# Optimization experiments

Measured on AMD Instinct MI355X. Metric: run time of the kernel, lower is better.

The kernel has to match this reference:

```python
import jax, jax.numpy as jnp
import numpy as np

NUM_HEADS = 8
SCALE = 1.0
BN_EPS = 1e-5


def _mlp1d(x, W1, g1, b1, W2):
    # Conv1d(k=1, bias=False) -> BatchNorm1d (training-mode batch stats) -> ReLU -> Conv1d(k=1, bias=False)
    h = jnp.einsum('oi,bil->bol', W1, x)
    mu = h.mean(axis=(0, 2), keepdims=True)
    var = h.var(axis=(0, 2), keepdims=True)  # biased var, as torch BN training
    h = (h - mu) * jax.lax.rsqrt(var + BN_EPS)
    h = jax.nn.relu(h * g1[None, :, None] + b1[None, :, None])
    return jnp.einsum('oi,bil->bol', W2, h)


def setup_inputs() -> dict:
    key = jax.random.key(0)
    ks = jax.random.split(key, 8)
    b, c, hh, ww = 64, 2048, 14, 14
    hid, out = 4096, 256
    d = {'x': jax.random.normal(ks[0], (b, c, hh, ww), jnp.float32)}

    def w(k, o, i):
        return jax.random.normal(k, (o, i), jnp.float32) * np.float32(1.0 / np.sqrt(i))

    i = 1
    for pre in ('p', 'pp', 'po'):  # proj, proj_pixel, proj_obj
        d[pre + 'W1'] = w(ks[i], hid, c); i += 1
        d[pre + 'G1'] = jnp.ones((hid,), jnp.float32)
        d[pre + 'B1'] = jnp.zeros((hid,), jnp.float32)
        d[pre + 'W2'] = w(ks[i], out, hid); i += 1
    return d


def reference(x, pW1, pG1, pB1, pW2, ppW1, ppG1, ppB1, ppW2, poW1, poG1, poB1, poW2):
    b, c, h, w = x.shape
    xf = x.reshape(b, c, h * w)                      # flatten(2)
    x_pool = xf.mean(axis=2, keepdims=True)          # adaptive_avg_pool2d(x, 1)
    z_g = _mlp1d(x_pool, pW1, pG1, pB1, pW2)         # [b, 256, 1]
    z_feat = _mlp1d(xf, ppW1, ppG1, ppB1, ppW2)      # [b, 256, hw]
    # F.normalize(dim=1) with eps=1e-12, then /scale
    nrm = jnp.maximum(jnp.linalg.norm(z_feat, axis=1, keepdims=True), 1e-12)
    attn = (z_feat / nrm) / SCALE
    attn = attn.reshape(b, NUM_HEADS, -1, h * w)     # [b, nh, 256/nh, hw]
    attn = jax.nn.softmax(attn, axis=-1)
    x4 = xf.reshape(b, NUM_HEADS, c // NUM_HEADS, h * w)
    # torch.matmul(x, obj_attn.transpose(3, 2)) : [b,nh,c/nh,hw] @ [b,nh,hw,q]
    obj_val = jnp.einsum('bnkl,bnql->bnkq', x4, attn).reshape(b, c, -1)  # [b, c, 256/nh]
    obj_val = _mlp1d(obj_val, poW1, poG1, poB1, poW2)                    # [b, 256, 32]
    return z_g, obj_val
```

## Files before the change

### kernel.cpp

```cpp
#include <hip/hip_runtime.h>
#include <hip/hip_bf16.h>

using bf16 = __hip_bfloat16;
typedef __bf16 bf16x8v __attribute__((ext_vector_type(8)));
typedef float f32x4 __attribute__((ext_vector_type(4)));

#define BN_EPS 1e-5f

__device__ __forceinline__ void stval(float* p, float v) { *p = v; }
__device__ __forceinline__ void stval(bf16* p, float v)  { *p = __float2bfloat16(v); }

__device__ __forceinline__ void gload_lds16(const void* g, void* l) {
    __builtin_amdgcn_global_load_lds(
        (const __attribute__((address_space(1))) unsigned int*)g,
        (__attribute__((address_space(3))) unsigned int*)l,
        16, 0, 0);
}

__device__ __forceinline__ int xcd_swz(int orig, int nwg) {
    int q = nwg >> 3, r = nwg & 7;
    int xcd = orig & 7, idx = orig >> 3;
    return (xcd < r ? xcd * (q + 1) : r * (q + 1) + (xcd - r) * q) + idx;
}

template<typename TC>
__global__ __launch_bounds__(512, 2) void mfma_tn8(
    const bf16* __restrict__ A, const bf16* __restrict__ B, TC* __restrict__ C,
    int M, int N, int K, float* __restrict__ ps, float* __restrict__ pq)
{
    __shared__ char lds[131072];
    const int NT = K >> 6;
    const int tid = threadIdx.x;
    const int lane = tid & 63;
    const int wv = tid >> 6;
    const int wm = wv >> 2;
    const int wn = wv & 3;

    const int nbx = gridDim.x;
    int flat = blockIdx.y * nbx + blockIdx.x;
    const int cpx = (nbx * gridDim.y) >> 3;
    flat = (flat & 7) * cpx + (flat >> 3);
    const int mtile = flat / nbx;
    const long m0 = (long)mtile * 256;
    const long n0 = (long)(flat % nbx) * 256;

    const int trow = tid >> 3;
    const int ks = (((tid & 7) ^ ((tid >> 3) & 7)) << 3);
    const bf16* Arow0 = A + (m0 + trow) * (long)K + ks;
    const bf16* Brow0 = B + (n0 + trow) * (long)K + ks;
    char* ldsA = (char*)lds + tid * 16;
    char* ldsB = (char*)lds + 32768 + tid * 16;

    auto stage_a = [&](int bbuf, int kt) {
        const bf16* g = Arow0 + ((long)kt << 6);
        char* d = ldsA + (bbuf << 16);
        gload_lds16(g, d);
        gload_lds16(g + ((long)K << 6),  d + 8192);
        gload_lds16(g + ((long)K << 7),  d + 16384);
        gload_lds16(g + 192L * (long)K,  d + 24576);
    };
    auto stage_b = [&](int bbuf, int kt) {
        const bf16* g = Brow0 + ((long)kt << 6);
        char* d = ldsB + (bbuf << 16);
        gload_lds16(g, d);
        gload_lds16(g + ((long)K << 6),  d + 8192);
        gload_lds16(g + ((long)K << 7),  d + 16384);
        gload_lds16(g + 192L * (long)K,  d + 24576);
    };

    const int fr = lane & 15, fc = lane >> 4;
    const int ca0 = ((fc ^ (fr & 7)) << 4);
    const int ca1 = (((4 + fc) ^ (fr & 7)) << 4);

    f32x4 acc[8][4];
#pragma unroll
    for (int m = 0; m < 8; ++m)
#pragma unroll
        for (int n = 0; n < 4; ++n) acc[m][n] = (f32x4){0.f, 0.f, 0.f, 0.f};

    stage_a(0, 0); stage_b(0, 0); stage_a(1, 1); stage_b(1, 1);

    for (int T = 0; T < NT; ++T) {
        const int bb = T & 1;
        const char* Ard = (const char*)lds + (bb << 16) + (wm * 128 + fr) * 128;
        const char* Brd = (const char*)lds + (bb << 16) + 32768 + (wn * 64 + fr) * 128;

        if (T == 0)          { asm volatile("s_waitcnt vmcnt(8)" ::: "memory"); }
        else if (T < NT - 1) { asm volatile("s_waitcnt vmcnt(4)" ::: "memory"); }
        else                 { asm volatile("s_waitcnt vmcnt(0)" ::: "memory"); }
        __builtin_amdgcn_s_barrier();
        __builtin_amdgcn_sched_barrier(0);

        bf16x8v a0[8], a1[8];
#pragma unroll
        for (int m = 0; m < 8; ++m) {
            a0[m] = *(const bf16x8v*)(Ard + m * 2048 + ca0);
            a1[m] = *(const bf16x8v*)(Ard + m * 2048 + ca1);
        }
        bf16x8v b00 = *(const bf16x8v*)(Brd + ca0);
        bf16x8v b01 = *(const bf16x8v*)(Brd + ca1);
        bf16x8v b10 = *(const bf16x8v*)(Brd + 2048 + ca0);
        bf16x8v b11 = *(const bf16x8v*)(Brd + 2048 + ca1);

        if (T >= 1 && T + 1 < NT) stage_b(bb ^ 1, T + 1);

        __builtin_amdgcn_s_setprio(1);
#pragma unroll
        for (int m = 0; m < 8; ++m) {
            acc[m][0] = __builtin_amdgcn_mfma_f32_16x16x32_bf16(a0[m], b00, acc[m][0], 0, 0, 0);
            acc[m][0] = __builtin_amdgcn_mfma_f32_16x16x32_bf16(a1[m], b01, acc[m][0], 0, 0, 0);
            acc[m][1] = __builtin_amdgcn_mfma_f32_16x16x32_bf16(a0[m], b10, acc[m][1], 0, 0, 0);
            acc[m][1] = __builtin_amdgcn_mfma_f32_16x16x32_bf16(a1[m], b11, acc[m][1], 0, 0, 0);
        }
        __builtin_amdgcn_s_setprio(0);

        __builtin_amdgcn_s_barrier();
        __builtin_amdgcn_sched_barrier(0);

        bf16x8v b20 = *(const bf16x8v*)(Brd + 2 * 2048 + ca0);
        bf16x8v b21 = *(const bf16x8v*)(Brd + 2 * 2048 + ca1);
        bf16x8v b30 = *(const bf16x8v*)(Brd + 3 * 2048 + ca0);
        bf16x8v b31 = *(const bf16x8v*)(Brd + 3 * 2048 + ca1);

        if (T + 2 < NT) stage_a(bb, T + 2);

        __builtin_amdgcn_s_setprio(1);
#pragma unroll
        for (int m = 0; m < 8; ++m) {
            acc[m][2] = __builtin_amdgcn_mfma_f32_16x16x32_bf16(a0[m], b20, acc[m][2], 0, 0, 0);
            acc[m][2] = __builtin_amdgcn_mfma_f32_16x16x32_bf16(a1[m], b21, acc[m][2], 0, 0, 0);
            acc[m][3] = __builtin_amdgcn_mfma_f32_16x16x32_bf16(a0[m], b30, acc[m][3], 0, 0, 0);
            acc[m][3] = __builtin_amdgcn_mfma_f32_16x16x32_bf16(a1[m], b31, acc[m][3], 0, 0, 0);
        }
        __builtin_amdgcn_s_setprio(0);
    }

#pragma unroll
    for (int m = 0; m < 8; ++m) {
        long gr = m0 + wm * 128 + m * 16 + fc * 4;
#pragma unroll
        for (int n = 0; n < 4; ++n) {
            long gc = n0 + wn * 64 + n * 16 + fr;
            TC* cp = C + gr * N + gc;
#pragma unroll
            for (int r = 0; r < 4; ++r) stval(cp + (long)r * N, acc[m][n][r]);
        }
    }

    if (ps != nullptr) {
        __syncthreads();
        float* red = (float*)lds;
        float cs[4], cq[4];
#pragma unroll
        for (int n = 0; n < 4; ++n) {
            float s = 0.f, q = 0.f;
#pragma unroll
            for (int m = 0; m < 8; ++m)
#pragma unroll
                for (int r = 0; r < 4; ++r) {
                    float v = __bfloat162float(__float2bfloat16(acc[m][n][r]));
                    s += v; q += v * v;
                }
            s += __shfl_xor(s, 16, 64); s += __shfl_xor(s, 32, 64);
            q += __shfl_xor(q, 16, 64); q += __shfl_xor(q, 32, 64);
            cs[n] = s; cq[n] = q;
        }
        if (fc == 0) {
#pragma unroll
            for (int n = 0; n < 4; ++n) {
                red[wv * 64 + n * 16 + fr] = cs[n];
                red[512 + wv * 64 + n * 16 + fr] = cq[n];
            }
        }
        __syncthreads();
        if (tid < 256) {
            int c = tid, wnn = c >> 6, idx = c & 63;
            float s = red[wnn * 64 + idx] + red[(4 + wnn) * 64 + idx];
            float q = red[512 + wnn * 64 + idx] + red[512 + (4 + wnn) * 64 + idx];
            ps[(long)mtile * N + n0 + c] = s;
            pq[(long)mtile * N + n0 + c] = q;
        }
    }
}

template<typename TC>
__global__ __launch_bounds__(256) void mfma_tn(
    const bf16* __restrict__ A, const bf16* __restrict__ B, TC* __restrict__ C,
    int M, int N, int K, float* __restrict__ ps, float* __restrict__ pq)
{
    __shared__ alignas(16) unsigned short As[128 * 32];
    __shared__ alignas(16) unsigned short Bs[128 * 32];

    const int tid = threadIdx.x;
    const int l = tid & 63;
    const int nwg = gridDim.x * gridDim.y;
    int s = xcd_swz(blockIdx.y * gridDim.x + blockIdx.x, nwg);
    const int by = s / gridDim.x, bx = s % gridDim.x;
    const long m0 = (long)by * 128;
    const long n0 = (long)bx * 128;
    const int wr = (tid >> 7) & 1;
    const int wc = (tid >> 6) & 1;

    const int off0 = tid * 16;
    const int row0 = off0 >> 6;
    const int kp0  = (off0 >> 4) & 3;
    const bf16* Ag0 = A + (m0 + row0) * (long)K + kp0 * 8;
    const bf16* Ag1 = A + (m0 + row0 + 64) * (long)K + kp0 * 8;
    const bf16* Bg0 = B + (n0 + row0) * (long)K + kp0 * 8;
    const bf16* Bg1 = B + (n0 + row0 + 64) * (long)K + kp0 * 8;
    char* Asl0 = (char*)As + off0;
    char* Asl1 = (char*)As + off0 + 4096;
    char* Bsl0 = (char*)Bs + off0;
    char* Bsl1 = (char*)Bs + off0 + 4096;

    f32x4 acc[4][4];
#pragma unroll
    for (int m = 0; m < 4; ++m)
#pragma unroll
        for (int n = 0; n < 4; ++n) acc[m][n] = (f32x4){0.f, 0.f, 0.f, 0.f};

    const int fr = l & 15;
    const int fc = l >> 4;
    int aoff[4], boff[4];
#pragma unroll
    for (int m = 0; m < 4; ++m) aoff[m] = ((wr * 64 + m * 16 + fr) * 4 + fc) * 16;
#pragma unroll
    for (int n = 0; n < 4; ++n) boff[n] = ((wc * 64 + n * 16 + fr) * 4 + fc) * 16;

    for (int k0 = 0; k0 < K; k0 += 32) {
        gload_lds16(Ag0 + k0, Asl0);
        gload_lds16(Ag1 + k0, Asl1);
        gload_lds16(Bg0 + k0, Bsl0);
        gload_lds16(Bg1 + k0, Bsl1);
        __syncthreads();

        bf16x8v af[4], bfr[4];
#pragma unroll
        for (int m = 0; m < 4; ++m) af[m]  = *(const bf16x8v*)((const char*)As + aoff[m]);
#pragma unroll
        for (int n = 0; n < 4; ++n) bfr[n] = *(const bf16x8v*)((const char*)Bs + boff[n]);
#pragma unroll
        for (int m = 0; m < 4; ++m)
#pragma unroll
            for (int n = 0; n < 4; ++n)
                acc[m][n] = __builtin_amdgcn_mfma_f32_16x16x32_bf16(af[m], bfr[n], acc[m][n], 0, 0, 0);
        __syncthreads();
    }

#pragma unroll
    for (int m = 0; m < 4; ++m) {
        long gr = m0 + wr * 64 + m * 16 + fc * 4;
#pragma unroll
        for (int n = 0; n < 4; ++n) {
            long gc = n0 + wc * 64 + n * 16 + fr;
            TC* cp = C + gr * N + gc;
#pragma unroll
            for (int r = 0; r < 4; ++r) stval(cp + (long)r * N, acc[m][n][r]);
        }
    }

    if (ps != nullptr) {
        float* red = (float*)As;
        float cs[4], cq[4];
#pragma unroll
        for (int n = 0; n < 4; ++n) {
            float s2 = 0.f, q2 = 0.f;
#pragma unroll
            for (int m = 0; m < 4; ++m)
#pragma unroll
                for (int r = 0; r < 4; ++r) {
                    float v = __bfloat162float(__float2bfloat16(acc[m][n][r]));
                    s2 += v; q2 += v * v;
                }
            s2 += __shfl_xor(s2, 16, 64); s2 += __shfl_xor(s2, 32, 64);
            q2 += __shfl_xor(q2, 16, 64); q2 += __shfl_xor(q2, 32, 64);
            cs[n] = s2; cq[n] = q2;
        }
        if (fc == 0) {
#pragma unroll
            for (int n = 0; n < 4; ++n) {
                int c = wc * 64 + n * 16 + fr;
                red[wr * 128 + c] = cs[n];
                red[256 + wr * 128 + c] = cq[n];
            }
        }
        __syncthreads();
        if (tid < 128) {
            float sv = red[tid] + red[128 + tid];
            float qv = red[256 + tid] + red[384 + tid];
            ps[(long)by * N + n0 + tid] = sv;
            pq[(long)by * N + n0 + tid] = qv;
        }
    }
}

__global__ __launch_bounds__(256) void mfma_tn_skbn(
    const bf16* __restrict__ A, const bf16* __restrict__ B, float* __restrict__ Cp,
    int M, int N, int K, int KCH, const float* __restrict__ ta, const float* __restrict__ tc)
{
    __shared__ alignas(16) unsigned short As[128 * 32];
    __shared__ alignas(16) unsigned short Bs[128 * 32];

    const int tid = threadIdx.x;
    const int l = tid & 63;
    const int gxy = gridDim.x * gridDim.y;
    const int nwg = gxy * gridDim.z;
    int s = xcd_swz((blockIdx.z * gridDim.y + blockIdx.y) * gridDim.x + blockIdx.x, nwg);
    const int bz = s / gxy;
    const int rem = s % gxy;
    const int by = rem / gridDim.x, bx = rem % gridDim.x;
    const long m0 = (long)by * 128;
    const long n0 = (long)bx * 128;
    const int wr = (tid >> 7) & 1;
    const int wc = (tid >> 6) & 1;
    const int ksrt = bz * KCH;

    const int off0 = tid * 16;
    const int row0 = off0 >> 6;
    const int kp0  = (off0 >> 4) & 3;
    const bf16* Ag0 = A + (m0 + row0) * (long)K + kp0 * 8 + ksrt;
    const bf16* Ag1 = A + (m0 + row0 + 64) * (long)K + kp0 * 8 + ksrt;
    const bf16* Bg0 = B + (n0 + row0) * (long)K + kp0 * 8 + ksrt;
    const bf16* Bg1 = B + (n0 + row0 + 64) * (long)K + kp0 * 8 + ksrt;
    char* Asl0 = (char*)As + off0;
    char* Asl1 = (char*)As + off0 + 4096;
    char* Bsl0 = (char*)Bs + off0;
    char* Bsl1 = (char*)Bs + off0 + 4096;

    f32x4 acc[4][4];
#pragma unroll
    for (int m = 0; m < 4; ++m)
#pragma unroll
        for (int n = 0; n < 4; ++n) acc[m][n] = (f32x4){0.f, 0.f, 0.f, 0.f};

    const int fr = l & 15;
    const int fc = l >> 4;
    int aoff[4], boff[4];
#pragma unroll
    for (int m = 0; m < 4; ++m) aoff[m] = ((wr * 64 + m * 16 + fr) * 4 + fc) * 16;
#pragma unroll
    for (int n = 0; n < 4; ++n) boff[n] = ((wc * 64 + n * 16 + fr) * 4 + fc) * 16;

    for (int k0 = 0; k0 < KCH; k0 += 32) {
        gload_lds16(Bg0 + k0, Bsl0);
        gload_lds16(Bg1 + k0, Bsl1);

        union { bf16 h[8]; uint4 u; } r0, r1;
        r0.u = *(const uint4*)(Ag0 + k0);
        r1.u = *(const uint4*)(Ag1 + k0);
        const int kb = ksrt + k0 + kp0 * 8;
        float4 av0 = *(const float4*)(ta + kb);
        float4 av1 = *(const float4*)(ta + kb + 4);
        float4 cv0 = *(const float4*)(tc + kb);
        float4 cv1 = *(const float4*)(tc + kb + 4);
        float av[8] = {av0.x, av0.y, av0.z, av0.w, av1.x, av1.y, av1.z, av1.w};
        float cv[8] = {cv0.x, cv0.y, cv0.z, cv0.w, cv1.x, cv1.y, cv1.z, cv1.w};
#pragma unroll
        for (int j = 0; j < 8; ++j) {
            float v = fmaxf(fmaf(av[j], __bfloat162float(r0.h[j]), cv[j]), 0.f);
            r0.h[j] = __float2bfloat16(v);
            v = fmaxf(fmaf(av[j], __bfloat162float(r1.h[j]), cv[j]), 0.f);
            r1.h[j] = __float2bfloat16(v);
        }
        *(uint4*)Asl0 = r0.u;
        *(uint4*)Asl1 = r1.u;
        __syncthreads();

        bf16x8v af[4], bfr[4];
#pragma unroll
        for (int m = 0; m < 4; ++m) af[m]  = *(const bf16x8v*)((const char*)As + aoff[m]);
#pragma unroll
        for (int n = 0; n < 4; ++n) bfr[n] = *(const bf16x8v*)((const char*)Bs + boff[n]);
#pragma unroll
        for (int m = 0; m < 4; ++m)
#pragma unroll
            for (int n = 0; n < 4; ++n)
                acc[m][n] = __builtin_amdgcn_mfma_f32_16x16x32_bf16(af[m], bfr[n], acc[m][n], 0, 0, 0);
        __syncthreads();
    }

    float* Cb = Cp + (long)bz * M * N;
#pragma unroll
    for (int m = 0; m < 4; ++m) {
        long gr = m0 + wr * 64 + m * 16 + fc * 4;
#pragma unroll
        for (int n = 0; n < 4; ++n) {
            long gc = n0 + wc * 64 + n * 16 + fr;
            float* cp = Cb + gr * N + gc;
#pragma unroll
            for (int r = 0; r < 4; ++r) cp[(long)r * N] = acc[m][n][r];
        }
    }
}

__global__ __launch_bounds__(256) void objmm_k(
    const bf16* __restrict__ attnP, const bf16* __restrict__ xP, bf16* __restrict__ objinT)
{
    __shared__ alignas(16) unsigned short As[32 * 32];
    __shared__ alignas(16) unsigned short Bs[256 * 32];
    const int tid = threadIdx.x, lane = tid & 63, wv = tid >> 6;
    const int b = blockIdx.x >> 3, h = blockIdx.x & 7;
    const bf16* Ab = attnP + ((long)(b * 256 + h * 32)) * 224;
    const bf16* Bb = xP + ((long)(b * 2048 + h * 256)) * 224;
    const int fr = lane & 15, fc = lane >> 4;
    const int srow = tid >> 2, schk = tid & 3;

    f32x4 acc[2][4];
#pragma unroll
    for (int m = 0; m < 2; ++m)
#pragma unroll
        for (int n = 0; n < 4; ++n) acc[m][n] = (f32x4){0.f, 0.f, 0.f, 0.f};

    for (int k0 = 0; k0 < 224; k0 += 32) {
        if (wv < 2)
            gload_lds16(Ab + (long)srow * 224 + schk * 8 + k0, (char*)As + tid * 16);
#pragma unroll
        for (int j = 0; j < 4; ++j)
            gload_lds16(Bb + (long)(j * 64 + srow) * 224 + schk * 8 + k0,
                        (char*)Bs + j * 4096 + tid * 16);
        __syncthreads();

        bf16x8v af[2], bfr[4];
#pragma unroll
        for (int m = 0; m < 2; ++m)
            af[m] = *(const bf16x8v*)((const char*)As + (m * 16 + fr) * 64 + fc * 16);
#pragma unroll
        for (int n = 0; n < 4; ++n)
            bfr[n] = *(const bf16x8v*)((const char*)Bs + (wv * 64 + n * 16 + fr) * 64 + fc * 16);
#pragma unroll
        for (int m = 0; m < 2; ++m)
#pragma unroll
            for (int n = 0; n < 4; ++n)
                acc[m][n] = __builtin_amdgcn_mfma_f32_16x16x32_bf16(af[m], bfr[n], acc[m][n], 0, 0, 0);
        __syncthreads();
    }

#pragma unroll
    for (int m = 0; m < 2; ++m) {
        long gr = (long)b * 32 + m * 16 + fc * 4;
#pragma unroll
        for (int n = 0; n < 4; ++n) {
            long gc = (long)h * 256 + wv * 64 + n * 16 + fr;
            bf16* cp = objinT + gr * 2048 + gc;
#pragma unroll
            for (int r = 0; r < 4; ++r) cp[(long)r * 2048] = __float2bfloat16(acc[m][n][r]);
        }
    }
}

__global__ __launch_bounds__(256) void foldnorm_k(const float* __restrict__ p,
    float* __restrict__ z, float* __restrict__ invn)
{
    int j = blockIdx.x * 4 + (threadIdx.x >> 6);
    int lane = threadIdx.x & 63;
    long off = (long)j * 256 + lane * 4;
    float4 a = *(const float4*)(p + off);
    float4 b = *(const float4*)(p + 3211264L + off);
    float4 c = *(const float4*)(p + 2 * 3211264L + off);
    float4 d = *(const float4*)(p + 3 * 3211264L + off);
    float4 s;
    s.x = (a.x + b.x) + (c.x + d.x);
    s.y = (a.y + b.y) + (c.y + d.y);
    s.z = (a.z + b.z) + (c.z + d.z);
    s.w = (a.w + b.w) + (c.w + d.w);
    *(float4*)(z + off) = s;
    float q = s.x * s.x + s.y * s.y + s.z * s.z + s.w * s.w;
#pragma unroll
    for (int off2 = 32; off2; off2 >>= 1) q += __shfl_xor(q, off2, 64);
    if (lane == 0) invn[j] = 1.f / fmaxf(sqrtf(q), 1e-12f);
}

__global__ __launch_bounds__(256) void foldout_k(const float* __restrict__ p, float* __restrict__ out)
{
    int o = blockIdx.x * 256 + threadIdx.x;
    int b = o >> 13, rem = o & 8191, q = rem >> 5, tt = rem & 31;
    long base = ((long)(b * 32 + tt)) * 256 + q;
    float s = 0.f;
#pragma unroll
    for (int z = 0; z < 8; ++z) s += p[(long)z * 524288 + base];
    out[o] = s;
}

__global__ __launch_bounds__(256) void convert4_k(
    const float* __restrict__ w1, const float* __restrict__ w2,
    const float* __restrict__ w3, const float* __restrict__ w4,
    bf16* __restrict__ o1, bf16* __restrict__ o2,
    bf16* __restrict__ o3, bf16* __restrict__ o4)
{
    const long L1 = 8388608, L2 = 1048576;
    long i = ((long)blockIdx.x * 256 + threadIdx.x) * 8;
    const float* src; bf16* dst; long e;
    if (i < L1)                { src = w1; dst = o1; e = i; }
    else if (i < L1 + L2)      { src = w2; dst = o2; e = i - L1; }
    else if (i < 2*L1 + L2)    { src = w3; dst = o3; e = i - L1 - L2; }
    else if (i < 2*L1 + 2*L2)  { src = w4; dst = o4; e = i - 2*L1 - L2; }
    else return;
    float4 v0 = *(const float4*)(src + e);
    float4 v1 = *(const float4*)(src + e + 4);
    union { bf16 h[8]; uint4 u; } r;
    r.h[0] = __float2bfloat16(v0.x); r.h[1] = __float2bfloat16(v0.y);
    r.h[2] = __float2bfloat16(v0.z); r.h[3] = __float2bfloat16(v0.w);
    r.h[4] = __float2bfloat16(v1.x); r.h[5] = __float2bfloat16(v1.y);
    r.h[6] = __float2bfloat16(v1.z); r.h[7] = __float2bfloat16(v1.w);
    *(uint4*)(dst + e) = r.u;
}

__global__ __launch_bounds__(256) void packx2_k(const float* __restrict__ x,
    bf16* __restrict__ XT, bf16* __restrict__ xP, float* __restrict__ xpT)
{
    __shared__ unsigned short tile[196 * 66 + 4];
    __shared__ float pp[64];
    const int t = threadIdx.x;
    const int b = blockIdx.y, c0 = blockIdx.x * 64;
    const int wvi = t >> 6, lane = t & 63;

    for (int p = 0; p < 16; ++p) {
        int c = p * 4 + wvi;
        const float* row = x + ((long)b * 2048 + c0 + c) * 196;
        float v0 = row[lane];
        float v1 = row[lane + 64];
        float v2 = row[lane + 128];
        float v3 = (lane < 4) ? row[lane + 192] : 0.f;
        bf16 h0 = __float2bfloat16(v0);
        bf16 h1 = __float2bfloat16(v1);
        bf16 h2 = __float2bfloat16(v2);
        bf16 h3 = __float2bfloat16(v3);
        tile[lane * 66 + c]         = *(unsigned short*)&h0;
        tile[(lane + 64) * 66 + c]  = *(unsigned short*)&h1;
        tile[(lane + 128) * 66 + c] = *(unsigned short*)&h2;
        if (lane < 4) tile[(lane + 192) * 66 + c] = *(unsigned short*)&h3;
        float s = v0 + v1 + v2 + v3;
#pragma unroll
        for (int off = 32; off; off >>= 1) s += __shfl_xor(s, off, 64);
        if (lane == 0) pp[c] = s;
    }
    __syncthreads();
    if (t < 64) xpT[(c0 + t) * 64 + b] = pp[t] * (1.f / 196.f);

    for (int u = t; u < 196 * 8; u += 256) {
        int l = u >> 3, cc = u & 7;
        const unsigned short* sp = &tile[l * 66 + cc * 8];
        uint4 r;
        r.x = *(const unsigned int*)(sp);
        r.y = *(const unsigned int*)(sp + 2);
        r.z = *(const unsigned int*)(sp + 4);
        r.w = *(const unsigned int*)(sp + 6);
        *(uint4*)(&XT[((long)b * 196 + l) * 2048 + c0 + cc * 8]) = r;
    }

    for (int u = t; u < 64 * 28; u += 256) {
        int c = u / 28, ch = u % 28;
        int l0 = ch * 8;
        union { unsigned short h[8]; uint4 v; } r;
#pragma unroll
        for (int e = 0; e < 8; ++e) {
            int ll = l0 + e;
            r.h[e] = (ll < 196) ? tile[ll * 66 + c] : (unsigned short)0;
        }
        *(uint4*)(xP + ((long)b * 2048 + c0 + c) * 224 + l0) = r.v;
    }
}

__global__ __launch_bounds__(256) void colstat2_k(const float* __restrict__ ps, const float* __restrict__ pq,
    int P, float invN, const float* __restrict__ g, const float* __restrict__ be,
    float* __restrict__ ta, float* __restrict__ tc)
{
    int c = blockIdx.x * 256 + threadIdx.x;
    float s = 0.f, q = 0.f;
    for (int p = 0; p < P; ++p) { s += ps[(long)p * 4096 + c]; q += pq[(long)p * 4096 + c]; }
    float mu  = s * invN;
    float var = q * invN - mu * mu;
    float a   = g[c] * rsqrtf(var + BN_EPS);
    ta[c] = a;
    tc[c] = be[c] - mu * a;
}

__global__ __launch_bounds__(256) void softmax2_k(const float* __restrict__ z,
    const float* __restrict__ invn, bf16* __restrict__ attnP)
{
    int row  = blockIdx.x * 4 + (threadIdx.x >> 6);
    int lane = threadIdx.x & 63;
    int b = row >> 8, q = row & 255;
    float v[4];
    float mx = -INFINITY;
#pragma unroll
    for (int i = 0; i < 4; ++i) {
        int l = lane + 64 * i;
        if (l < 196) {
            int j = b * 196 + l;
            v[i] = z[(long)j * 256 + q] * invn[j];
        } else v[i] = -INFINITY;
        mx = fmaxf(mx, v[i]);
    }
#pragma unroll
    for (int off = 32; off; off >>= 1) mx = fmaxf(mx, __shfl_xor(mx, off, 64));
    float s = 0.f;
#pragma unroll
    for (int i = 0; i < 4; ++i) {
        v[i] = (lane + 64 * i < 196) ? __expf(v[i] - mx) : 0.f;
        s += v[i];
    }
#pragma unroll
    for (int off = 32; off; off >>= 1) s += __shfl_xor(s, off, 64);
    float is = 1.f / s;
    bf16* rp = attnP + (long)row * 224;
#pragma unroll
    for (int i = 0; i < 4; ++i) {
        int l = lane + 64 * i;
        if (l < 196) rp[l] = __float2bfloat16(v[i] * is);
        else if (l < 224) rp[l] = __float2bfloat16(0.f);
    }
}

template<bool TRANS>
__global__ __launch_bounds__(256) void gemmsk_k(
    const float* __restrict__ A, const float* __restrict__ B, float* __restrict__ Cp,
    int M, int N, int K, int lda, int ldbk, int KCH,
    const float* __restrict__ tra, const float* __restrict__ trc)
{
    constexpr int BM = 64, BN = 64, BK = 16;
    __shared__ float As[BK][BM + 4];
    __shared__ float Bs[BK][BN + 4];

    const int tid = threadIdx.x;
    const int m0 = blockIdx.y * BM;
    const int ks = blockIdx.z * KCH;
    const int ke = min(K, ks + KCH);

    const int tIdm = tid / 16;
    const int tIdn = tid % 16;
    const int aK  = tid % BK;
    const int aM0 = tid / BK;
    const int bN  = tid % BN;
    const int bK0 = tid / BN;

    float acc[4][4];
#pragma unroll
    for (int u = 0; u < 4; ++u)
#pragma unroll
        for (int v = 0; v < 4; ++v) acc[u][v] = 0.f;

    for (int k0 = ks; k0 < ke; k0 += BK) {
#pragma unroll
        for (int i = 0; i < 4; ++i) {
            int m = aM0 + 16 * i;
            int gk = k0 + aK, gm = m0 + m;
            float v = 0.f;
            if (gk < ke && gm < M) v = A[(long)gm * lda + gk];
            As[aK][m] = v;
        }
#pragma unroll
        for (int i = 0; i < 4; ++i) {
            int kk = bK0 + 4 * i;
            int gk = k0 + kk;
            float v = 0.f;
            if (gk < ke && bN < N) {
                v = B[(long)gk * ldbk + bN];
                if (TRANS) v = fmaxf(tra[gk] * v + trc[gk], 0.f);
            }
            Bs[kk][bN] = v;
        }
        __syncthreads();
#pragma unroll
        for (int kk = 0; kk < BK; ++kk) {
            float a[4], b[4];
#pragma unroll
            for (int u = 0; u < 4; ++u) a[u] = As[kk][tIdm * 4 + u];
#pragma unroll
            for (int v = 0; v < 4; ++v) b[v] = Bs[kk][tIdn * 4 + v];
#pragma unroll
            for (int u = 0; u < 4; ++u)
#pragma unroll
                for (int v = 0; v < 4; ++v)
                    acc[u][v] = fmaf(a[u], b[v], acc[u][v]);
        }
        __syncthreads();
    }

    float* Cb = Cp + (long)blockIdx.z * M * N;
#pragma unroll
    for (int u = 0; u < 4; ++u) {
        int gm = m0 + tIdm * 4 + u;
        if (gm >= M) continue;
#pragma unroll
        for (int v = 0; v < 4; ++v) {
            int gn = tIdn * 4 + v;
            if (gn < N) Cb[(long)gm * N + gn] = acc[u][v];
        }
    }
}

__global__ __launch_bounds__(256) void skbn_k(const float* __restrict__ Cp,
    const float* __restrict__ g, const float* __restrict__ be,
    float* __restrict__ h1, float* __restrict__ ta, float* __restrict__ tc)
{
    int o = blockIdx.x * 4 + (threadIdx.x >> 6);
    int b = threadIdx.x & 63;
    float s = 0.f;
#pragma unroll
    for (int p = 0; p < 16; ++p) s += Cp[(long)p * 262144 + o * 64 + b];
    h1[o * 64 + b] = s;
    float s1 = s, s2 = s * s;
#pragma unroll
    for (int off = 32; off; off >>= 1) {
        s1 += __shfl_down(s1, off, 64);
        s2 += __shfl_down(s2, off, 64);
    }
    if (b == 0) {
        float mu  = s1 * (1.f / 64.f);
        float var = s2 * (1.f / 64.f) - mu * mu;
        float a   = g[o] * rsqrtf(var + BN_EPS);
        ta[o] = a;
        tc[o] = be[o] - mu * a;
    }
}

__global__ __launch_bounds__(256) void skreduce_k(const float* __restrict__ Cp, int P, long MN,
    int Nn, int ldm, int ldn, float* __restrict__ out)
{
    long i = (long)blockIdx.x * 256 + threadIdx.x;
    if (i >= MN) return;
    float s = 0.f;
    for (int p = 0; p < P; ++p) s += Cp[(long)p * MN + i];
    int m = (int)(i / Nn), n = (int)(i % Nn);
    out[(long)m * ldm + (long)n * ldn] = s;
}

extern "C" void kernel_launch(void* const* d_in, const int* in_sizes, int n_in,
                              void* d_out, int out_size, void* d_ws, size_t ws_size,
                              hipStream_t stream)
{
    const float* x    = (const float*)d_in[0];
    const float* pW1  = (const float*)d_in[1];
    const float* pG1  = (const float*)d_in[2];
    const float* pB1  = (const float*)d_in[3];
    const float* pW2  = (const float*)d_in[4];
    const float* ppW1 = (const float*)d_in[5];
    const float* ppG1 = (const float*)d_in[6];
    const float* ppB1 = (const float*)d_in[7];
    const float* ppW2 = (const float*)d_in[8];
    const float* poW1 = (const float*)d_in[9];
    const float* poG1 = (const float*)d_in[10];
    const float* poB1 = (const float*)d_in[11];
    const float* poW2 = (const float*)d_in[12];
    float* out = (float*)d_out;
    (void)in_sizes; (void)n_in; (void)out_size; (void)ws_size;

    char* w = (char*)d_ws;
    auto alloc = [&](size_t bytes) -> char* {
        char* p = w; w += (bytes + 255) & ~(size_t)255; return p;
    };
    bf16* ppW1b = (bf16*)alloc((size_t)4096 * 2048 * 2);
    bf16* ppW2b = (bf16*)alloc((size_t)256 * 4096 * 2);
    bf16* poW1b = (bf16*)alloc((size_t)4096 * 2048 * 2);
    bf16* poW2b = (bf16*)alloc((size_t)256 * 4096 * 2);
    char* region1 = alloc((size_t)12544 * 2048 * 2);
    bf16*  XT     = (bf16*)region1;
    float* skpG2  = (float*)region1;
    bf16*  attnP  = (bf16*)region1;
    bf16*  objinT = (bf16*)(region1 + 12845056);
    bf16*  hobjT  = (bf16*)(region1 + 12845056 + 8388608);
    bf16* xP     = (bf16*)alloc((size_t)64 * 2048 * 224 * 2);
    bf16* hfeatT = (bf16*)alloc((size_t)12544 * 4096 * 2);
    float* zfeatT = (float*)alloc((size_t)12544 * 256 * 4);
    float* ps    = (float*)alloc((size_t)49 * 4096 * 4);
    float* pq    = (float*)alloc((size_t)49 * 4096 * 4);
    float* invn  = (float*)alloc((size_t)12544 * 4);
    float* a2    = (float*)alloc(4096 * 4);
    float* c2    = (float*)alloc(4096 * 4);
    float* a3    = (float*)alloc(4096 * 4);
    float* c3    = (float*)alloc(4096 * 4);
    float* xpT   = (float*)alloc((size_t)2048 * 64 * 4);
    float* h1    = (float*)alloc((size_t)4096 * 64 * 4);
    float* a1    = (float*)alloc(4096 * 4);
    float* c1    = (float*)alloc(4096 * 4);
    float* skp1  = (float*)alloc((size_t)16 * 4096 * 64 * 4);
    float* skp2  = (float*)alloc((size_t)32 * 256 * 64 * 4);
    float* skp5  = (float*)alloc((size_t)8 * 2048 * 256 * 4);

    convert4_k<<<9216, 256, 0, stream>>>(ppW1, ppW2, poW1, poW2, ppW1b, ppW2b, poW1b, poW2b);
    packx2_k<<<dim3(32, 64), 256, 0, stream>>>(x, XT, xP, xpT);

    gemmsk_k<false><<<dim3(1, 64, 16), 256, 0, stream>>>(
        pW1, xpT, skp1, 4096, 64, 2048, 2048, 64, 128, nullptr, nullptr);
    skbn_k<<<1024, 256, 0, stream>>>(skp1, pG1, pB1, h1, a1, c1);
    gemmsk_k<true><<<dim3(1, 4, 32), 256, 0, stream>>>(
        pW2, h1, skp2, 256, 64, 4096, 4096, 64, 128, a1, c1);
    skreduce_k<<<64, 256, 0, stream>>>(skp2, 32, (long)256 * 64, 64, 1, 256, out);

    mfma_tn8<bf16><<<dim3(16, 49), 512, 0, stream>>>(XT, ppW1b, hfeatT, 12544, 4096, 2048, ps, pq);
    colstat2_k<<<16, 256, 0, stream>>>(ps, pq, 49, 1.f / 12544.f, ppG1, ppB1, a2, c2);

    mfma_tn_skbn<<<dim3(2, 98, 4), 256, 0, stream>>>(
        hfeatT, ppW2b, skpG2, 12544, 256, 4096, 1024, a2, c2);
    foldnorm_k<<<3136, 256, 0, stream>>>(skpG2, zfeatT, invn);

    softmax2_k<<<4096, 256, 0, stream>>>(zfeatT, invn, attnP);

    objmm_k<<<512, 256, 0, stream>>>(attnP, xP, objinT);

    mfma_tn<bf16><<<dim3(32, 16), 256, 0, stream>>>(objinT, poW1b, hobjT, 2048, 4096, 2048, ps, pq);
    colstat2_k<<<16, 256, 0, stream>>>(ps, pq, 16, 1.f / 2048.f, poG1, poB1, a3, c3);

    mfma_tn_skbn<<<dim3(2, 16, 8), 256, 0, stream>>>(
        hobjT, poW2b, skp5, 2048, 256, 4096, 512, a3, c3);
    foldout_k<<<2048, 256, 0, stream>>>(skp5, out + 16384);
}
```

Measured before the change: 613.0 us.

## Split GEMM main loop into four quadrant phases with half-tile prefetch

Restructures the 256x256 MFMA GEMM inner loop into four phases, each working on half of the A rows and half of the B columns. Global-to-LDS prefetches are issued in half-tile chunks between phases, and barriers with waitcnt sit at each phase. Only half of the A fragments are held in registers at a time, which lowers register pressure. The intent is finer interleaving of memory traffic with MFMA work, at the cost of more barriers per iteration and a more complex hazard schedule that needs correct double-buffer synchronisation.

```diff
diff --git a/kernel.cpp b/kernel.cpp
--- a/kernel.cpp
+++ b/kernel.cpp
@@ -22,6 +22,8 @@
     int xcd = orig & 7, idx = orig >> 3;
     return (xcd < r ? xcd * (q + 1) : r * (q + 1) + (xcd - r) * q) + idx;
 }
+
+#define MFMA_BF16 __builtin_amdgcn_mfma_f32_16x16x32_bf16
 
 template<typename TC>
 __global__ __launch_bounds__(512, 2) void mfma_tn8(
@@ -51,21 +53,17 @@
     char* ldsA = (char*)lds + tid * 16;
     char* ldsB = (char*)lds + 32768 + tid * 16;
 
-    auto stage_a = [&](int bbuf, int kt) {
-        const bf16* g = Arow0 + ((long)kt << 6);
-        char* d = ldsA + (bbuf << 16);
+    auto stage_a_half = [&](int bbuf, int kt, int h) {
+        const bf16* g = Arow0 + (long)(h * 64) * K + ((long)kt << 6);
+        char* d = ldsA + (bbuf << 16) + h * 8192;
         gload_lds16(g, d);
-        gload_lds16(g + ((long)K << 6),  d + 8192);
-        gload_lds16(g + ((long)K << 7),  d + 16384);
-        gload_lds16(g + 192L * (long)K,  d + 24576);
+        gload_lds16(g + ((long)K << 7), d + 16384);
     };
-    auto stage_b = [&](int bbuf, int kt) {
-        const bf16* g = Brow0 + ((long)kt << 6);
-        char* d = ldsB + (bbuf << 16);
+    auto stage_b_half = [&](int bbuf, int kt, int h) {
+        const bf16* g = Brow0 + (long)(h * 128) * K + ((long)kt << 6);
+        char* d = ldsB + (bbuf << 16) + h * 16384;
         gload_lds16(g, d);
-        gload_lds16(g + ((long)K << 6),  d + 8192);
-        gload_lds16(g + ((long)K << 7),  d + 16384);
-        gload_lds16(g + 192L * (long)K,  d + 24576);
+        gload_lds16(g + ((long)K << 6), d + 8192);
     };
 
     const int fr = lane & 15, fc = lane >> 4;
@@ -78,61 +76,98 @@
 #pragma unroll
         for (int n = 0; n < 4; ++n) acc[m][n] = (f32x4){0.f, 0.f, 0.f, 0.f};
 
-    stage_a(0, 0); stage_b(0, 0); stage_a(1, 1); stage_b(1, 1);
+    stage_a_half(0, 0, 0); stage_a_half(0, 0, 1);
+    stage_b_half(0, 0, 0); stage_b_half(0, 0, 1);
+    stage_a_half(1, 1, 0); stage_a_half(1, 1, 1);
+    asm volatile("s_waitcnt vmcnt(4)" ::: "memory");
+    __builtin_amdgcn_s_barrier();
+    __builtin_amdgcn_sched_barrier(0);
 
     for (int T = 0; T < NT; ++T) {
         const int bb = T & 1;
         const char* Ard = (const char*)lds + (bb << 16) + (wm * 128 + fr) * 128;
         const char* Brd = (const char*)lds + (bb << 16) + 32768 + (wn * 64 + fr) * 128;
 
-        if (T == 0)          { asm volatile("s_waitcnt vmcnt(8)" ::: "memory"); }
-        else if (T < NT - 1) { asm volatile("s_waitcnt vmcnt(4)" ::: "memory"); }
-        else                 { asm volatile("s_waitcnt vmcnt(0)" ::: "memory"); }
+        bf16x8v a0[4], a1[4];
+        bf16x8v b00, b01, b10, b11, b20, b21, b30, b31;
+
+#pragma unroll
+        for (int i = 0; i < 4; ++i) {
+            a0[i] = *(const bf16x8v*)(Ard + i * 2048 + ca0);
+            a1[i] = *(const bf16x8v*)(Ard + i * 2048 + ca1);
+        }
+        b00 = *(const bf16x8v*)(Brd + ca0);
+        b01 = *(const bf16x8v*)(Brd + ca1);
+        b10 = *(const bf16x8v*)(Brd + 2048 + ca0);
+        b11 = *(const bf16x8v*)(Brd + 2048 + ca1);
+        if (T + 1 < NT) stage_b_half(bb ^ 1, T + 1, 0);
+        __builtin_amdgcn_s_barrier();
+        asm volatile("s_waitcnt lgkmcnt(0)" ::: "memory");
+        __builtin_amdgcn_sched_barrier(0);
+        __builtin_amdgcn_s_setprio(1);
+#pragma unroll
+        for (int i = 0; i < 4; ++i) {
+            acc[i][0] = MFMA_BF16(a0[i], b00, acc[i][0], 0, 0, 0);
+            acc[i][0] = MFMA_BF16(a1[i], b01, acc[i][0], 0, 0, 0);
+            acc[i][1] = MFMA_BF16(a0[i], b10, acc[i][1], 0, 0, 0);
+            acc[i][1] = MFMA_BF16(a1[i], b11, acc[i][1], 0, 0, 0);
+        }
+        __builtin_amdgcn_s_setprio(0);
+        __builtin_amdgcn_s_barrier();
+
+        b20 = *(const bf16x8v*)(Brd + 2 * 2048 + ca0);
+        b21 = *(const bf16x8v*)(Brd + 2 * 2048 + ca1);
+        b30 = *(const bf16x8v*)(Brd + 3 * 2048 + ca0);
+        b31 = *(const bf16x8v*)(Brd + 3 * 2048 + ca1);
+        if (T + 1 < NT) stage_b_half(bb ^ 1, T + 1, 1);
+        __builtin_amdgcn_s_barrier();
+        asm volatile("s_waitcnt lgkmcnt(0)" ::: "memory");
+        __builtin_amdgcn_sched_barrier(0);
+        __builtin_amdgcn_s_setprio(1);
+#pragma unroll
+        for (int i = 0; i < 4; ++i) {
+            acc[i][2] = MFMA_BF16(a0[i], b20, acc[i][2], 0, 0, 0);
+            acc[i][2] = MFMA_BF16(a1[i], b21, acc[i][2], 0, 0, 0);
+            acc[i][3] = MFMA_BF16(a0[i], b30, acc[i][3], 0, 0, 0);
+            acc[i][3] = MFMA_BF16(a1[i], b31, acc[i][3], 0, 0, 0);
+        }
+        __builtin_amdgcn_s_setprio(0);
+        __builtin_amdgcn_s_barrier();
+
+#pragma unroll
+        for (int i = 0; i < 4; ++i) {
+            a0[i] = *(const bf16x8v*)(Ard + (4 + i) * 2048 + ca0);
+            a1[i] = *(const bf16x8v*)(Ard + (4 + i) * 2048 + ca1);
+        }
+        if (T + 2 < NT) stage_a_half(bb, T + 2, 0);
+        __builtin_amdgcn_s_barrier();
+        asm volatile("s_waitcnt lgkmcnt(0)" ::: "memory");
+        __builtin_amdgcn_sched_barrier(0);
+        __builtin_amdgcn_s_setprio(1);
+#pragma unroll
+        for (int i = 0; i < 4; ++i) {
+            acc[4 + i][0] = MFMA_BF16(a0[i], b00, acc[4 + i][0], 0, 0, 0);
+            acc[4 + i][0] = MFMA_BF16(a1[i], b01, acc[4 + i][0], 0, 0, 0);
+            acc[4 + i][1] = MFMA_BF16(a0[i], b10, acc[4 + i][1], 0, 0, 0);
+            acc[4 + i][1] = MFMA_BF16(a1[i], b11, acc[4 + i][1], 0, 0, 0);
+        }
+        __builtin_amdgcn_s_setprio(0);
+        __builtin_amdgcn_s_barrier();
+
+        if (T + 2 < NT) stage_a_half(bb, T + 2, 1);
+        __builtin_amdgcn_s_setprio(1);
+#pragma unroll
+        for (int i = 0; i < 4; ++i) {
+            acc[4 + i][2] = MFMA_BF16(a0[i], b20, acc[4 + i][2], 0, 0, 0);
+            acc[4 + i][2] = MFMA_BF16(a1[i], b21, acc[4 + i][2], 0, 0, 0);
+            acc[4 + i][3] = MFMA_BF16(a0[i], b30, acc[4 + i][3], 0, 0, 0);
+            acc[4 + i][3] = MFMA_BF16(a1[i], b31, acc[4 + i][3], 0, 0, 0);
+        }
+        __builtin_amdgcn_s_setprio(0);
+        if (T + 2 < NT)      { asm volatile("s_waitcnt vmcnt(4)" ::: "memory"); }
+        else if (T + 1 < NT) { asm volatile("s_waitcnt vmcnt(0)" ::: "memory"); }
         __builtin_amdgcn_s_barrier();
         __builtin_amdgcn_sched_barrier(0);
-
-        bf16x8v a0[8], a1[8];
-#pragma unroll
-        for (int m = 0; m < 8; ++m) {
-            a0[m] = *(const bf16x8v*)(Ard + m * 2048 + ca0);
-            a1[m] = *(const bf16x8v*)(Ard + m * 2048 + ca1);
-        }
-        bf16x8v b00 = *(const bf16x8v*)(Brd + ca0);
-        bf16x8v b01 = *(const bf16x8v*)(Brd + ca1);
-        bf16x8v b10 = *(const bf16x8v*)(Brd + 2048 + ca0);
-        bf16x8v b11 = *(const bf16x8v*)(Brd + 2048 + ca1);
-
-        if (T >= 1 && T + 1 < NT) stage_b(bb ^ 1, T + 1);
-
-        __builtin_amdgcn_s_setprio(1);
-#pragma unroll
-        for (int m = 0; m < 8; ++m) {
-            acc[m][0] = __builtin_amdgcn_mfma_f32_16x16x32_bf16(a0[m], b00, acc[m][0], 0, 0, 0);
-            acc[m][0] = __builtin_amdgcn_mfma_f32_16x16x32_bf16(a1[m], b01, acc[m][0], 0, 0, 0);
-            acc[m][1] = __builtin_amdgcn_mfma_f32_16x16x32_bf16(a0[m], b10, acc[m][1], 0, 0, 0);
-            acc[m][1] = __builtin_amdgcn_mfma_f32_16x16x32_bf16(a1[m], b11, acc[m][1], 0, 0, 0);
-        }
-        __builtin_amdgcn_s_setprio(0);
-
-        __builtin_amdgcn_s_barrier();
-        __builtin_amdgcn_sched_barrier(0);
-
-        bf16x8v b20 = *(const bf16x8v*)(Brd + 2 * 2048 + ca0);
-        bf16x8v b21 = *(const bf16x8v*)(Brd + 2 * 2048 + ca1);
-        bf16x8v b30 = *(const bf16x8v*)(Brd + 3 * 2048 + ca0);
-        bf16x8v b31 = *(const bf16x8v*)(Brd + 3 * 2048 + ca1);
-
-        if (T + 2 < NT) stage_a(bb, T + 2);
-
-        __builtin_amdgcn_s_setprio(1);
-#pragma unroll
-        for (int m = 0; m < 8; ++m) {
-            acc[m][2] = __builtin_amdgcn_mfma_f32_16x16x32_bf16(a0[m], b20, acc[m][2], 0, 0, 0);
-            acc[m][2] = __builtin_amdgcn_mfma_f32_16x16x32_bf16(a1[m], b21, acc[m][2], 0, 0, 0);
-            acc[m][3] = __builtin_amdgcn_mfma_f32_16x16x32_bf16(a0[m], b30, acc[m][3], 0, 0, 0);
-            acc[m][3] = __builtin_amdgcn_mfma_f32_16x16x32_bf16(a1[m], b31, acc[m][3], 0, 0, 0);
-        }
-        __builtin_amdgcn_s_setprio(0);
     }
 
 #pragma unroll
@@ -243,7 +278,7 @@
         for (int m = 0; m < 4; ++m)
 #pragma unroll
             for (int n = 0; n < 4; ++n)
-                acc[m][n] = __builtin_amdgcn_mfma_f32_16x16x32_bf16(af[m], bfr[n], acc[m][n], 0, 0, 0);
+                acc[m][n] = MFMA_BF16(af[m], bfr[n], acc[m][n], 0, 0, 0);
         __syncthreads();
     }
 
@@ -375,7 +410,7 @@
         for (int m = 0; m < 4; ++m)
 #pragma unroll
             for (int n = 0; n < 4; ++n)
-                acc[m][n] = __builtin_amdgcn_mfma_f32_16x16x32_bf16(af[m], bfr[n], acc[m][n], 0, 0, 0);
+                acc[m][n] = MFMA_BF16(af[m], bfr[n], acc[m][n], 0, 0, 0);
         __syncthreads();
     }
 
@@ -431,7 +466,7 @@
         for (int m = 0; m < 2; ++m)
 #pragma unroll
             for (int n = 0; n < 4; ++n)
-                acc[m][n] = __builtin_amdgcn_mfma_f32_16x16x32_bf16(af[m], bfr[n], acc[m][n], 0, 0, 0);
+                acc[m][n] = MFMA_BF16(af[m], bfr[n], acc[m][n], 0, 0, 0);
         __syncthreads();
     }
 
```

New measurement: 637.4 us. 4.0% more time.
